# Kernel tuning notes

Hardware: AMD Instinct MI355X
Metric: run time of the kernel (lower is better)

The kernel has to match this reference:

```python
import jax, jax.numpy as jnp
import numpy as np

N_NODES = 50000
N_EDGES = 800000
D_IN = 512
D_OUT = 256

def setup_inputs() -> dict:
    key = jax.random.key(0)
    k1, k2, k3, k4, k5 = jax.random.split(key, 5)
    return {
        "inputs": jax.random.normal(k1, (N_NODES, D_IN), dtype=jnp.float32),
        "weights": jax.random.uniform(k2, (D_IN, D_OUT), dtype=jnp.float32, minval=-0.1, maxval=0.1),
        "bias": jnp.zeros((D_OUT,), dtype=jnp.float32),
        "edge_vals": jax.random.uniform(k3, (N_EDGES,), dtype=jnp.float32),
        "edge_row": jax.random.randint(k4, (N_EDGES,), 0, N_NODES),
        "edge_col": jax.random.randint(k5, (N_EDGES,), 0, N_NODES),
    }

def reference(inputs, weights, bias, edge_vals, edge_row, edge_col):
    # dense projection: [N, D_in] @ [D_in, D_out] -> [N, D_out]
    supports = inputs @ weights
    # sparse adjacency spmm in COO form: out[i] = sum_e vals[e] * supports[col[e]] for row[e] == i
    msgs = supports[edge_col] * edge_vals[:, None]  # [E, D_out]
    aggregated = jax.ops.segment_sum(msgs, edge_row, num_segments=inputs.shape[0])
    return aggregated + bias
```

## Files before the change

### kernel.cpp

```cpp
#include <hip/hip_runtime.h>

#define D_IN 512
#define D_OUT 256
#define BM 64
#define BK 32
#define LDK 40

typedef short short8 __attribute__((ext_vector_type(8)));
typedef float floatx4 __attribute__((ext_vector_type(4)));

static __device__ __forceinline__ unsigned short f2bf(float f) {
    unsigned u = __float_as_uint(f);
    u += 0x7FFF + ((u >> 16) & 1);
    return (unsigned short)(u >> 16);
}
static __device__ __forceinline__ float bf2f(unsigned short h) {
    return __uint_as_float((unsigned)h << 16);
}

#define CONV_BLOCKS 256
__global__ __launch_bounds__(512) void convert_and_zero(const float* __restrict__ W,
                                                        unsigned short* __restrict__ Wt,
                                                        int* __restrict__ cnt, int M) {
    int b = blockIdx.x;
    if (b < CONV_BLOCKS) {
        int t = b * 512 + threadIdx.x;
        int n = t >> 9;
        int k = t & 511;
        Wt[t] = f2bf(W[(size_t)k * D_OUT + n]);
    } else {
        int i = (b - CONV_BLOCKS) * 512 + threadIdx.x;
        if (i < M) cnt[i] = 0;
    }
}

__global__ __launch_bounds__(256) void hist_rows(const int* __restrict__ rows,
                                                 int* __restrict__ cnt, int E) {
    int e = blockIdx.x * 256 + threadIdx.x;
    if (e < E) atomicAdd(&cnt[rows[e]], 1);
}

#define SCAN_B 4096
__global__ __launch_bounds__(1024) void scan_blocks(const int* __restrict__ cnt,
                                                    int* __restrict__ ptr,
                                                    int* __restrict__ partials, int M) {
    __shared__ int wsum[16];
    const int t = threadIdx.x, lane = t & 63, wave = t >> 6;
    const int base = blockIdx.x * SCAN_B + t * 4;
    int4 v = make_int4(0, 0, 0, 0);
    if (base + 3 < M) v = *(const int4*)(cnt + base);
    else {
        if (base + 0 < M) v.x = cnt[base + 0];
        if (base + 1 < M) v.y = cnt[base + 1];
        if (base + 2 < M) v.z = cnt[base + 2];
        if (base + 3 < M) v.w = cnt[base + 3];
    }
    int s = v.x + v.y + v.z + v.w;
    int incl = s;
#pragma unroll
    for (int off = 1; off < 64; off <<= 1) {
        int x = __shfl_up(incl, off, 64);
        if (lane >= off) incl += x;
    }
    if (lane == 63) wsum[wave] = incl;
    __syncthreads();
    if (t == 0) {
        int run = 0;
#pragma unroll
        for (int w = 0; w < 16; ++w) { int x = wsum[w]; wsum[w] = run; run += x; }
        partials[blockIdx.x] = run;
    }
    __syncthreads();
    int e0 = wsum[wave] + (incl - s);
    int e1 = e0 + v.x, e2 = e1 + v.y, e3 = e2 + v.z;
    if (base + 3 < M) *(int4*)(ptr + base) = make_int4(e0, e1, e2, e3);
    else {
        if (base + 0 < M) ptr[base + 0] = e0;
        if (base + 1 < M) ptr[base + 1] = e1;
        if (base + 2 < M) ptr[base + 2] = e2;
        if (base + 3 < M) ptr[base + 3] = e3;
    }
}

__global__ __launch_bounds__(64) void scan_partials(int* __restrict__ partials,
                                                    int* __restrict__ ptr, int M, int nb) {
    const int t = threadIdx.x;
    int v = (t < nb) ? partials[t] : 0;
    int incl = v;
#pragma unroll
    for (int off = 1; off < 64; off <<= 1) {
        int x = __shfl_up(incl, off, 64);
        if (t >= off) incl += x;
    }
    if (t < nb) partials[t] = incl - v;
    if (t == 63) ptr[M] = incl;
}

__global__ __launch_bounds__(256) void add_offsets(int* __restrict__ ptr,
                                                   const int* __restrict__ partials,
                                                   int M) {
    int i = blockIdx.x * 256 + threadIdx.x;
    if (i < M) ptr[i] += partials[i >> 12];
}

__global__ __launch_bounds__(512, 4) void gemm_build(
    const float* __restrict__ A, const unsigned short* __restrict__ Wt,
    unsigned short* __restrict__ S, int M, int nGemm,
    const float* __restrict__ vals, const int* __restrict__ rows,
    const int* __restrict__ cols, int* __restrict__ ptr,
    int2* __restrict__ edges, int E) {
    __shared__ unsigned short As[BM * LDK];
    __shared__ unsigned short Bs[D_OUT * LDK];
    const int tid = threadIdx.x;

    if ((int)blockIdx.x >= nGemm) {
        int e = ((int)blockIdx.x - nGemm) * 512 + tid;
        if (e < E) {
            int r = rows[e];
            int pos = atomicAdd(&ptr[r], 1);
            edges[pos] = make_int2(cols[e], __float_as_int(vals[e]));
        }
        return;
    }

    const int lane = tid & 63;
    const int wave = tid >> 6;
    const int wn   = wave * 32;
    const int bm   = blockIdx.x * BM;
    const int l15  = lane & 15;
    const int quad = lane >> 4;

    const int am   = tid >> 3;
    const int ak4  = (tid & 7) * 4;
    const bool aval = (bm + am) < M;
    const float* aptr = A + (size_t)(aval ? bm + am : 0) * D_IN + ak4;
    const int aoff = am * LDK + ak4;

    const unsigned short* bptr[2];
    int boff[2];
#pragma unroll
    for (int i = 0; i < 2; ++i) {
        int item = tid + i * 512;
        int bn = item >> 2;
        int k8 = (item & 3) * 8;
        bptr[i] = Wt + (size_t)bn * D_IN + k8;
        boff[i] = bn * LDK + k8;
    }

    float4 aR = aval ? *(const float4*)aptr : make_float4(0.f, 0.f, 0.f, 0.f);
    short8 bR[2];
#pragma unroll
    for (int i = 0; i < 2; ++i) bR[i] = *(const short8*)(bptr[i]);

    floatx4 acc[4][2] = {};

    for (int k0 = 0; k0 < D_IN; k0 += BK) {
        ushort4 ab;
        ab.x = f2bf(aR.x); ab.y = f2bf(aR.y); ab.z = f2bf(aR.z); ab.w = f2bf(aR.w);
        *(ushort4*)(As + aoff) = ab;
#pragma unroll
        for (int i = 0; i < 2; ++i) *(short8*)(Bs + boff[i]) = bR[i];
        __syncthreads();

        if (k0 + BK < D_IN) {
            aR = aval ? *(const float4*)(aptr + k0 + BK)
                      : make_float4(0.f, 0.f, 0.f, 0.f);
#pragma unroll
            for (int i = 0; i < 2; ++i) bR[i] = *(const short8*)(bptr[i] + k0 + BK);
        }

        short8 af[4], bfr[2];
#pragma unroll
        for (int i = 0; i < 4; ++i)
            af[i] = *(const short8*)(As + (i * 16 + l15) * LDK + quad * 8);
#pragma unroll
        for (int j = 0; j < 2; ++j)
            bfr[j] = *(const short8*)(Bs + (wn + j * 16 + l15) * LDK + quad * 8);
#pragma unroll
        for (int i = 0; i < 4; ++i)
#pragma unroll
            for (int j = 0; j < 2; ++j)
                acc[i][j] = __builtin_amdgcn_mfma_f32_16x16x32_bf16(
                    af[i], bfr[j], acc[i][j], 0, 0, 0);
        __syncthreads();
    }

#pragma unroll
    for (int i = 0; i < 4; ++i) {
#pragma unroll
        for (int r = 0; r < 4; ++r) {
            int gm = bm + i * 16 + quad * 4 + r;
            if (gm < M) {
#pragma unroll
                for (int j = 0; j < 2; ++j)
                    S[(size_t)gm * D_OUT + wn + j * 16 + l15] = f2bf(acc[i][j][r]);
            }
        }
    }
}

__global__ __launch_bounds__(256) void spmm_rows(const unsigned short* __restrict__ S,
                                                 const int2* __restrict__ edges,
                                                 const int* __restrict__ ptr,
                                                 const float* __restrict__ bias,
                                                 float* __restrict__ out, int M) {
    const int row = blockIdx.x * 4 + (threadIdx.x >> 6);
    if (row >= M) return;
    const int lane = threadIdx.x & 63;
    float4 a0 = ((const float4*)bias)[lane];
    float4 a1 = make_float4(0.f, 0.f, 0.f, 0.f);
    const int beg = row ? ptr[row - 1] : 0;
    const int end = ptr[row];
    int j = beg;
    for (; j + 7 < end; j += 8) {
        int2 e0 = edges[j + 0], e1 = edges[j + 1], e2 = edges[j + 2], e3 = edges[j + 3];
        int2 e4 = edges[j + 4], e5 = edges[j + 5], e6 = edges[j + 6], e7 = edges[j + 7];
        ushort4 s0 = ((const ushort4*)(S + (size_t)e0.x * D_OUT))[lane];
        ushort4 s1 = ((const ushort4*)(S + (size_t)e1.x * D_OUT))[lane];
        ushort4 s2 = ((const ushort4*)(S + (size_t)e2.x * D_OUT))[lane];
        ushort4 s3 = ((const ushort4*)(S + (size_t)e3.x * D_OUT))[lane];
        ushort4 s4 = ((const ushort4*)(S + (size_t)e4.x * D_OUT))[lane];
        ushort4 s5 = ((const ushort4*)(S + (size_t)e5.x * D_OUT))[lane];
        ushort4 s6 = ((const ushort4*)(S + (size_t)e6.x * D_OUT))[lane];
        ushort4 s7 = ((const ushort4*)(S + (size_t)e7.x * D_OUT))[lane];
        float v0 = __int_as_float(e0.y), v1 = __int_as_float(e1.y);
        float v2 = __int_as_float(e2.y), v3 = __int_as_float(e3.y);
        float v4 = __int_as_float(e4.y), v5 = __int_as_float(e5.y);
        float v6 = __int_as_float(e6.y), v7 = __int_as_float(e7.y);
        a0.x += v0 * bf2f(s0.x) + v2 * bf2f(s2.x) + v4 * bf2f(s4.x) + v6 * bf2f(s6.x);
        a0.y += v0 * bf2f(s0.y) + v2 * bf2f(s2.y) + v4 * bf2f(s4.y) + v6 * bf2f(s6.y);
        a0.z += v0 * bf2f(s0.z) + v2 * bf2f(s2.z) + v4 * bf2f(s4.z) + v6 * bf2f(s6.z);
        a0.w += v0 * bf2f(s0.w) + v2 * bf2f(s2.w) + v4 * bf2f(s4.w) + v6 * bf2f(s6.w);
        a1.x += v1 * bf2f(s1.x) + v3 * bf2f(s3.x) + v5 * bf2f(s5.x) + v7 * bf2f(s7.x);
        a1.y += v1 * bf2f(s1.y) + v3 * bf2f(s3.y) + v5 * bf2f(s5.y) + v7 * bf2f(s7.y);
        a1.z += v1 * bf2f(s1.z) + v3 * bf2f(s3.z) + v5 * bf2f(s5.z) + v7 * bf2f(s7.z);
        a1.w += v1 * bf2f(s1.w) + v3 * bf2f(s3.w) + v5 * bf2f(s5.w) + v7 * bf2f(s7.w);
    }
    for (; j + 3 < end; j += 4) {
        int2 e0 = edges[j], e1 = edges[j + 1], e2 = edges[j + 2], e3 = edges[j + 3];
        ushort4 s0 = ((const ushort4*)(S + (size_t)e0.x * D_OUT))[lane];
        ushort4 s1 = ((const ushort4*)(S + (size_t)e1.x * D_OUT))[lane];
        ushort4 s2 = ((const ushort4*)(S + (size_t)e2.x * D_OUT))[lane];
        ushort4 s3 = ((const ushort4*)(S + (size_t)e3.x * D_OUT))[lane];
        float v0 = __int_as_float(e0.y), v1 = __int_as_float(e1.y);
        float v2 = __int_as_float(e2.y), v3 = __int_as_float(e3.y);
        a0.x += v0 * bf2f(s0.x) + v2 * bf2f(s2.x);
        a0.y += v0 * bf2f(s0.y) + v2 * bf2f(s2.y);
        a0.z += v0 * bf2f(s0.z) + v2 * bf2f(s2.z);
        a0.w += v0 * bf2f(s0.w) + v2 * bf2f(s2.w);
        a1.x += v1 * bf2f(s1.x) + v3 * bf2f(s3.x);
        a1.y += v1 * bf2f(s1.y) + v3 * bf2f(s3.y);
        a1.z += v1 * bf2f(s1.z) + v3 * bf2f(s3.z);
        a1.w += v1 * bf2f(s1.w) + v3 * bf2f(s3.w);
    }
    for (; j < end; ++j) {
        int2 e = edges[j];
        float v = __int_as_float(e.y);
        ushort4 s = ((const ushort4*)(S + (size_t)e.x * D_OUT))[lane];
        a0.x += v * bf2f(s.x);
        a0.y += v * bf2f(s.y);
        a0.z += v * bf2f(s.z);
        a0.w += v * bf2f(s.w);
    }
    a0.x += a1.x; a0.y += a1.y; a0.z += a1.z; a0.w += a1.w;
    floatx4 res = {a0.x, a0.y, a0.z, a0.w};
    __builtin_nontemporal_store(res, (floatx4*)(out + (size_t)row * D_OUT) + lane);
}

extern "C" void kernel_launch(void* const* d_in, const int* in_sizes, int n_in,
                              void* d_out, int out_size, void* d_ws, size_t ws_size,
                              hipStream_t stream) {
    const float* inputs    = (const float*)d_in[0];
    const float* weights   = (const float*)d_in[1];
    const float* bias      = (const float*)d_in[2];
    const float* edge_vals = (const float*)d_in[3];
    const int*   edge_row  = (const int*)d_in[4];
    const int*   edge_col  = (const int*)d_in[5];
    float* out = (float*)d_out;

    const int M = in_sizes[0] / D_IN;
    const int E = in_sizes[3];

    char* ws = (char*)d_ws;
    unsigned short* S  = (unsigned short*)ws;
    unsigned short* Wt = (unsigned short*)(ws + (size_t)M * D_OUT * 2);
    int2* edges        = (int2*)((char*)Wt + (size_t)D_OUT * D_IN * 2);
    int*  ptr          = (int*)((char*)edges + (size_t)E * 8);
    int*  cnt          = ptr + ((M + 4) & ~3);
    int*  partials     = cnt + M;

    int nzero = (M + 511) / 512;
    convert_and_zero<<<CONV_BLOCKS + nzero, 512, 0, stream>>>(weights, Wt, cnt, M);

    hist_rows<<<(E + 255) / 256, 256, 0, stream>>>(edge_row, cnt, E);
    int nb = (M + SCAN_B - 1) / SCAN_B;
    scan_blocks<<<nb, 1024, 0, stream>>>(cnt, ptr, partials, M);
    scan_partials<<<1, 64, 0, stream>>>(partials, ptr, M, nb);
    add_offsets<<<(M + 255) / 256, 256, 0, stream>>>(ptr, partials, M);

    int nGemm  = (M + BM - 1) / BM;
    int nBuild = (E + 511) / 512;
    gemm_build<<<nGemm + nBuild, 512, 0, stream>>>(inputs, Wt, S, M, nGemm,
                                                   edge_vals, edge_row, edge_col,
                                                   ptr, edges, E);

    spmm_rows<<<(M + 3) / 4, 256, 0, stream>>>(S, edges, ptr, bias, out, M);
}
```

Measured before the change: 311.1 us.

## Pre-convert inputs to bf16, stream GEMM tiles via global_load_lds, fuse scan passes

A new prep kernel converts the fp32 input matrix to bf16 in a padded workspace buffer. A new 128x128-tile GEMM uses direct global-to-LDS loads (global_load_lds) when the workspace is large enough, and otherwise falls back to the old register-staged GEMM. The three-kernel scan becomes a single kernel with decoupled look-back over ready-flagged partials, and the histogram kernel is vectorized to four edges per thread. This aims to cut launch count and GEMM load overhead, at the cost of an extra full pass over the inputs for conversion and a serial look-back spin across blocks.

```diff
diff --git a/kernel.cpp b/kernel.cpp
--- a/kernel.cpp
+++ b/kernel.cpp
@@ -2,12 +2,11 @@
 
 #define D_IN 512
 #define D_OUT 256
-#define BM 64
 #define BK 32
-#define LDK 40
 
 typedef short short8 __attribute__((ext_vector_type(8)));
 typedef float floatx4 __attribute__((ext_vector_type(4)));
+typedef unsigned int u32;
 
 static __device__ __forceinline__ unsigned short f2bf(float f) {
     unsigned u = __float_as_uint(f);
@@ -18,33 +17,66 @@
     return __uint_as_float((unsigned)h << 16);
 }
 
-#define CONV_BLOCKS 256
-__global__ __launch_bounds__(512) void convert_and_zero(const float* __restrict__ W,
-                                                        unsigned short* __restrict__ Wt,
-                                                        int* __restrict__ cnt, int M) {
+static __device__ __forceinline__ void gload16(const void* g, void* l) {
+    __builtin_amdgcn_global_load_lds(
+        (const __attribute__((address_space(1))) u32*)g,
+        (__attribute__((address_space(3))) u32*)l, 16, 0, 0);
+}
+
+__global__ __launch_bounds__(512) void prep(const float* __restrict__ A,
+                                            unsigned short* __restrict__ A16,
+                                            const float* __restrict__ W,
+                                            unsigned short* __restrict__ Wt,
+                                            int* __restrict__ cnt,
+                                            int M, int NA, int NZ) {
     int b = blockIdx.x;
-    if (b < CONV_BLOCKS) {
-        int t = b * 512 + threadIdx.x;
+    if (b < NA) {
+        size_t e = (size_t)b * 4096 + threadIdx.x * 8;
+        int row = (int)(e >> 9);
+        short8 o;
+        if (row < M) {
+            float4 lo = *(const float4*)(A + e);
+            float4 hi = *(const float4*)(A + e + 4);
+            o[0] = (short)f2bf(lo.x); o[1] = (short)f2bf(lo.y);
+            o[2] = (short)f2bf(lo.z); o[3] = (short)f2bf(lo.w);
+            o[4] = (short)f2bf(hi.x); o[5] = (short)f2bf(hi.y);
+            o[6] = (short)f2bf(hi.z); o[7] = (short)f2bf(hi.w);
+        } else {
+            o = (short8){0, 0, 0, 0, 0, 0, 0, 0};
+        }
+        *(short8*)(A16 + e) = o;
+    } else if (b < NA + 256) {
+        int t = (b - NA) * 512 + threadIdx.x;
         int n = t >> 9;
         int k = t & 511;
         Wt[t] = f2bf(W[(size_t)k * D_OUT + n]);
     } else {
-        int i = (b - CONV_BLOCKS) * 512 + threadIdx.x;
-        if (i < M) cnt[i] = 0;
+        int i = (b - NA - 256) * 512 + threadIdx.x;
+        if (i < NZ) cnt[i] = 0;
     }
 }
 
 __global__ __launch_bounds__(256) void hist_rows(const int* __restrict__ rows,
                                                  int* __restrict__ cnt, int E) {
-    int e = blockIdx.x * 256 + threadIdx.x;
-    if (e < E) atomicAdd(&cnt[rows[e]], 1);
+    int e0 = (blockIdx.x * 256 + threadIdx.x) * 4;
+    if (e0 + 3 < E) {
+        int4 r = *(const int4*)(rows + e0);
+        atomicAdd(&cnt[r.x], 1);
+        atomicAdd(&cnt[r.y], 1);
+        atomicAdd(&cnt[r.z], 1);
+        atomicAdd(&cnt[r.w], 1);
+    } else {
+        for (int e = e0; e < E; ++e) atomicAdd(&cnt[rows[e]], 1);
+    }
 }
 
 #define SCAN_B 4096
+#define SCAN_READY (1 << 30)
 __global__ __launch_bounds__(1024) void scan_blocks(const int* __restrict__ cnt,
                                                     int* __restrict__ ptr,
                                                     int* __restrict__ partials, int M) {
     __shared__ int wsum[16];
+    __shared__ int s_off;
     const int t = threadIdx.x, lane = t & 63, wave = t >> 6;
     const int base = blockIdx.x * SCAN_B + t * 4;
     int4 v = make_int4(0, 0, 0, 0);
@@ -68,11 +100,18 @@
         int run = 0;
 #pragma unroll
         for (int w = 0; w < 16; ++w) { int x = wsum[w]; wsum[w] = run; run += x; }
-        partials[blockIdx.x] = run;
+        atomicExch(&partials[blockIdx.x], run | SCAN_READY);
+        int off = 0;
+        for (int j = 0; j < (int)blockIdx.x; ++j) {
+            int pv;
+            do { pv = atomicAdd(&partials[j], 0); } while (!(pv & SCAN_READY));
+            off += pv & ~SCAN_READY;
+        }
+        s_off = off;
     }
     __syncthreads();
-    int e0 = wsum[wave] + (incl - s);
-    int e1 = e0 + v.x, e2 = e1 + v.y, e3 = e2 + v.z;
+    int g = s_off + wsum[wave] + (incl - s);
+    int e0 = g, e1 = e0 + v.x, e2 = e1 + v.y, e3 = e2 + v.z;
     if (base + 3 < M) *(int4*)(ptr + base) = make_int4(e0, e1, e2, e3);
     else {
         if (base + 0 < M) ptr[base + 0] = e0;
@@ -82,35 +121,91 @@
     }
 }
 
-__global__ __launch_bounds__(64) void scan_partials(int* __restrict__ partials,
-                                                    int* __restrict__ ptr, int M, int nb) {
-    const int t = threadIdx.x;
-    int v = (t < nb) ? partials[t] : 0;
-    int incl = v;
-#pragma unroll
-    for (int off = 1; off < 64; off <<= 1) {
-        int x = __shfl_up(incl, off, 64);
-        if (t >= off) incl += x;
-    }
-    if (t < nb) partials[t] = incl - v;
-    if (t == 63) ptr[M] = incl;
-}
-
-__global__ __launch_bounds__(256) void add_offsets(int* __restrict__ ptr,
-                                                   const int* __restrict__ partials,
-                                                   int M) {
-    int i = blockIdx.x * 256 + threadIdx.x;
-    if (i < M) ptr[i] += partials[i >> 12];
-}
-
-__global__ __launch_bounds__(512, 4) void gemm_build(
+__global__ __launch_bounds__(512, 4) void gemm_build_lds(
+    const unsigned short* __restrict__ A16, const unsigned short* __restrict__ Wt,
+    unsigned short* __restrict__ S, int M, int nGemm,
+    const float* __restrict__ vals, const int* __restrict__ rows,
+    const int* __restrict__ cols, int* __restrict__ ptr,
+    int2* __restrict__ edges, int E) {
+    __shared__ unsigned short lds[8192];
+    const int bid = blockIdx.x;
+    const int tid = threadIdx.x;
+
+    if (bid >= nGemm) {
+        int e = (bid - nGemm) * 512 + tid;
+        if (e < E) {
+            int r = rows[e];
+            int pos = atomicAdd(&ptr[r], 1);
+            edges[pos] = make_int2(cols[e], __float_as_int(vals[e]));
+        }
+        return;
+    }
+
+    const int bm   = (bid >> 1) * 128;
+    const int bn   = (bid & 1) * 128;
+    const int lane = tid & 63;
+    const int wave = tid >> 6;
+    const int l15  = lane & 15;
+    const int quad = lane >> 4;
+    const int wm   = (wave >> 2) * 64;
+    const int wn   = (wave & 3) * 32;
+
+    const unsigned short* aSrc = A16 + (size_t)(bm + (tid & 127)) * D_IN + (tid >> 7) * 8;
+    const unsigned short* bSrc = Wt  + (size_t)(bn + (tid & 127)) * D_IN + (tid >> 7) * 8;
+    unsigned short* aDst = lds + tid * 8;
+    unsigned short* bDst = lds + 4096 + tid * 8;
+
+    floatx4 acc[4][2] = {};
+
+#define STAGE(K0) { gload16(aSrc + (K0), aDst); gload16(bSrc + (K0), bDst); }
+
+    STAGE(0);
+#pragma unroll
+    for (int t = 0; t < 16; ++t) {
+        __syncthreads();
+
+        short8 af[4], bfr[2];
+#pragma unroll
+        for (int i = 0; i < 4; ++i)
+            af[i] = *(const short8*)(lds + (quad * 128 + wm + i * 16 + l15) * 8);
+#pragma unroll
+        for (int j = 0; j < 2; ++j)
+            bfr[j] = *(const short8*)(lds + 4096 + (quad * 128 + wn + j * 16 + l15) * 8);
+#pragma unroll
+        for (int i = 0; i < 4; ++i)
+#pragma unroll
+            for (int j = 0; j < 2; ++j)
+                acc[i][j] = __builtin_amdgcn_mfma_f32_16x16x32_bf16(
+                    af[i], bfr[j], acc[i][j], 0, 0, 0);
+
+        __syncthreads();
+        if (t < 15) STAGE((t + 1) * BK);
+    }
+#undef STAGE
+
+#pragma unroll
+    for (int i = 0; i < 4; ++i) {
+#pragma unroll
+        for (int r = 0; r < 4; ++r) {
+            int gm = bm + wm + i * 16 + quad * 4 + r;
+            if (gm < M) {
+#pragma unroll
+                for (int j = 0; j < 2; ++j)
+                    S[(size_t)gm * D_OUT + bn + wn + j * 16 + l15] = f2bf(acc[i][j][r]);
+            }
+        }
+    }
+}
+
+#define LDK 40
+__global__ __launch_bounds__(512, 4) void gemm_build_reg(
     const float* __restrict__ A, const unsigned short* __restrict__ Wt,
     unsigned short* __restrict__ S, int M, int nGemm,
     const float* __restrict__ vals, const int* __restrict__ rows,
     const int* __restrict__ cols, int* __restrict__ ptr,
     int2* __restrict__ edges, int E) {
-    __shared__ unsigned short As[BM * LDK];
-    __shared__ unsigned short Bs[D_OUT * LDK];
+    __shared__ unsigned short As[64 * LDK];
+    __shared__ unsigned short Bs[256 * LDK];
     const int tid = threadIdx.x;
 
     if ((int)blockIdx.x >= nGemm) {
@@ -126,7 +221,7 @@
     const int lane = tid & 63;
     const int wave = tid >> 6;
     const int wn   = wave * 32;
-    const int bm   = blockIdx.x * BM;
+    const int bm   = blockIdx.x * 64;
     const int l15  = lane & 15;
     const int quad = lane >> 4;
 
@@ -280,29 +375,44 @@
 
     const int M = in_sizes[0] / D_IN;
     const int E = in_sizes[3];
+    const int MP = ((M + 127) / 128) * 128;
+
+    const size_t szS   = (size_t)M * D_OUT * 2;
+    const size_t szWt  = (size_t)D_OUT * D_IN * 2;
+    const size_t szA16 = (size_t)MP * D_IN * 2;
+    const size_t szE   = (size_t)E * 8;
+    const size_t szTail = ((size_t)((M + 4) & ~3) + M + 64) * 4;
+    const bool mainPath = ws_size >= szS + szWt + szA16 + szE + szTail;
 
     char* ws = (char*)d_ws;
-    unsigned short* S  = (unsigned short*)ws;
-    unsigned short* Wt = (unsigned short*)(ws + (size_t)M * D_OUT * 2);
-    int2* edges        = (int2*)((char*)Wt + (size_t)D_OUT * D_IN * 2);
-    int*  ptr          = (int*)((char*)edges + (size_t)E * 8);
-    int*  cnt          = ptr + ((M + 4) & ~3);
-    int*  partials     = cnt + M;
-
-    int nzero = (M + 511) / 512;
-    convert_and_zero<<<CONV_BLOCKS + nzero, 512, 0, stream>>>(weights, Wt, cnt, M);
-
-    hist_rows<<<(E + 255) / 256, 256, 0, stream>>>(edge_row, cnt, E);
-    int nb = (M + SCAN_B - 1) / SCAN_B;
-    scan_blocks<<<nb, 1024, 0, stream>>>(cnt, ptr, partials, M);
-    scan_partials<<<1, 64, 0, stream>>>(partials, ptr, M, nb);
-    add_offsets<<<(M + 255) / 256, 256, 0, stream>>>(ptr, partials, M);
-
-    int nGemm  = (M + BM - 1) / BM;
+    unsigned short* S   = (unsigned short*)ws;
+    unsigned short* Wt  = (unsigned short*)(ws + szS);
+    unsigned short* A16 = (unsigned short*)(ws + szS + szWt);
+    int2* edges  = (int2*)(ws + szS + szWt + (mainPath ? szA16 : 0));
+    int*  ptr    = (int*)((char*)edges + szE);
+    int*  cnt    = ptr + ((M + 4) & ~3);
+    int*  partials = cnt + M;
+
+    int NA = mainPath ? (int)((szA16 / 2) / 4096) : 0;
+    int NZ = M + 16;
+    prep<<<NA + 256 + (NZ + 511) / 512, 512, 0, stream>>>(inputs, A16, weights, Wt,
+                                                          cnt, M, NA, NZ);
+
+    hist_rows<<<(E + 1023) / 1024, 256, 0, stream>>>(edge_row, cnt, E);
+    scan_blocks<<<(M + SCAN_B - 1) / SCAN_B, 1024, 0, stream>>>(cnt, ptr, partials, M);
+
     int nBuild = (E + 511) / 512;
-    gemm_build<<<nGemm + nBuild, 512, 0, stream>>>(inputs, Wt, S, M, nGemm,
-                                                   edge_vals, edge_row, edge_col,
-                                                   ptr, edges, E);
+    if (mainPath) {
+        int nGemm = (MP / 128) * 2;
+        gemm_build_lds<<<nGemm + nBuild, 512, 0, stream>>>(A16, Wt, S, M, nGemm,
+                                                           edge_vals, edge_row, edge_col,
+                                                           ptr, edges, E);
+    } else {
+        int nGemm = (M + 63) / 64;
+        gemm_build_reg<<<nGemm + nBuild, 512, 0, stream>>>(inputs, Wt, S, M, nGemm,
+                                                           edge_vals, edge_row, edge_col,
+                                                           ptr, edges, E);
+    }
 
     spmm_rows<<<(M + 3) / 4, 256, 0, stream>>>(S, edges, ptr, bias, out, M);
 }
```

Result: slower. 349.6 us (+12.4%).
